# Kernel tuning notes

Measured on AMD Instinct MI355X. Metric: run time of the kernel, lower is better.

## Reference

```python
import jax, jax.numpy as jnp
import numpy as np

CLIP_MIN = 0.0
CLIP_MAX = 1.0
B, T, F, E, CD = 64, 48, 128, 64, 32


def setup_inputs() -> dict:
    key = jax.random.key(0)
    ks = jax.random.split(key, 8)
    return {
        "input_x": jax.random.uniform(ks[0], (B, T, F), dtype=jnp.float32),
        "mask": jax.random.randint(ks[1], (B, T, F), 0, 2, dtype=jnp.int32),
        "embed0": jax.random.normal(ks[2], (F, E), dtype=jnp.float32) * 0.1,
        "embed1": jax.random.normal(ks[3], (F, E), dtype=jnp.float32) * 0.1,
        "embed_missing": jax.random.normal(ks[4], (F, E), dtype=jnp.float32) * 0.1,
        "attention_f_w": jax.random.normal(ks[5], (F, E), dtype=jnp.float32) * 0.1,
        "attention_f_b": jnp.zeros((F,), dtype=jnp.float32),
        "compress_w": jax.random.normal(ks[6], (2 * E, CD), dtype=jnp.float32) * 0.1,
    }


def reference(input_x, mask, embed0, embed1, embed_missing, attention_f_w, attention_f_b, compress_w):
    b, t, f = input_x.shape
    # new_mask: feature observed anywhere in time -> [b, 1, f, 1] (broadcasts over time)
    m = (jnp.sum(mask, axis=-2) != 0).astype(input_x.dtype)[:, None, :, None]
    x = input_x[..., None]  # [b, t, f, 1]
    # interval embedding c: [b, t, f, e]
    c0 = (x - m * CLIP_MIN) * embed0
    c1 = (m * CLIP_MAX - x) * embed1
    c = (c0 + c1) / (CLIP_MAX - CLIP_MIN) + (1.0 - m) * embed_missing
    # pairwise scores: sum_e c_i * c_j * w_i + b_i  (avoids [b,t,f,f,e] materialization)
    scores = jnp.einsum("btie,btje->btij", c * attention_f_w, c) + attention_f_b[:, None]
    scores = jnp.clip(scores, -5.0, 5.0)
    off_diag = 1.0 - jnp.eye(f, dtype=c.dtype)
    masked_exps = jnp.exp(scores) * off_diag
    attn = masked_exps / (jnp.sum(masked_exps, axis=-1, keepdims=True) + 1e-8)  # [b,t,f,f]
    # weighted aggregation: sum_j attn_ij * (c_i * c_j) = c_i * (attn @ c)_i
    agg = c * jnp.einsum("btij,btje->btie", attn, c)
    a = jax.nn.relu(jnp.concatenate([c, agg], axis=-1))  # [b,t,f,2e]
    out = jnp.einsum("btfk,kd->btfd", a, compress_w)
    return out.reshape(b, t, f * compress_w.shape[-1])
```

## Files before the change

kernel.cpp:

```cpp
#include <hip/hip_runtime.h>

#define NB 64
#define NT 48
#define NF 128
#define NE 64
#define NCD 32

#define LOG2E 1.4426950408889634f

typedef __attribute__((ext_vector_type(8))) short bf16x8;
typedef __attribute__((ext_vector_type(4))) float f32x4;
typedef __attribute__((ext_vector_type(2))) uint u32x2;

#define WS_MFLAG 0
#define WS_DB    32768
#define WS_E1B   49152
#define WS_EMB   65536
#define WS_WLB   81920
#define WS_WT    98304
#define WS_BL    106496

__device__ __forceinline__ ushort f2bf(float x) {
    union { float f; uint u; } v; v.f = x;
    uint r = v.u + 0x7fffu + ((v.u >> 16) & 1u);
    return (ushort)(r >> 16);
}
__device__ __forceinline__ uint pk_bf16(float lo, float hi) {
    uint r; asm("v_cvt_pk_bf16_f32 %0, %1, %2" : "=v"(r) : "v"(lo), "v"(hi)); return r;
}
__device__ __forceinline__ float bflo(uint u) { union { uint u; float f; } v; v.u = u << 16; return v.f; }
__device__ __forceinline__ float bfhi(uint u) { union { uint u; float f; } v; v.u = u & 0xffff0000u; return v.f; }
__device__ __forceinline__ float exp2i(float x) { float r; asm("v_exp_f32 %0, %1" : "=v"(r) : "v"(x)); return r; }
__device__ __forceinline__ float rcpi(float x)  { float r; asm("v_rcp_f32 %0, %1" : "=v"(r) : "v"(x)); return r; }

#define TRR(dst, addr, IMM) \
    asm volatile("ds_read_b64_tr_b16 %0, %1 offset:" IMM : "=v"(dst) : "v"(addr))
#define PLSWAP(a, b) asm("v_permlane32_swap_b32 %0, %1" : "+v"(a), "+v"(b))

#define AGG_ISSUE(CR, TB, O0, O1, O2, O3, O4, O5, O6, O7) \
    TRR(CR[0], TB, O0); TRR(CR[1], TB, O1); \
    TRR(CR[2], TB, O2); TRR(CR[3], TB, O3); \
    TRR(CR[4], TB, O4); TRR(CR[5], TB, O5); \
    TRR(CR[6], TB, O6); TRR(CR[7], TB, O7); \
    __builtin_amdgcn_sched_barrier(0);

#define AGG_CONSUME(CR, PF, AG) { \
    union { u32x2 d[2]; bf16x8 v; } q0, q1, q2, q3; \
    q0.d[0] = CR[0]; q0.d[1] = CR[1]; q1.d[0] = CR[2]; q1.d[1] = CR[3]; \
    q2.d[0] = CR[4]; q2.d[1] = CR[5]; q3.d[0] = CR[6]; q3.d[1] = CR[7]; \
    AG[0] = __builtin_amdgcn_mfma_f32_16x16x32_bf16(q0.v, PF, AG[0], 0, 0, 0); \
    AG[1] = __builtin_amdgcn_mfma_f32_16x16x32_bf16(q1.v, PF, AG[1], 0, 0, 0); \
    AG[2] = __builtin_amdgcn_mfma_f32_16x16x32_bf16(q2.v, PF, AG[2], 0, 0, 0); \
    AG[3] = __builtin_amdgcn_mfma_f32_16x16x32_bf16(q3.v, PF, AG[3], 0, 0, 0); }

#define PF_BUILD(PF, PP, KS) { \
    uint X0 = PP[4*(KS)], X1 = PP[4*(KS)+1], X2 = PP[4*(KS)+2], X3 = PP[4*(KS)+3]; \
    PLSWAP(X0, X2); PLSWAP(X1, X3); \
    PF.u[0] = X0; PF.u[1] = X1; PF.u[2] = X2; PF.u[3] = X3; }

#define LGKM_WAIT(N) \
    asm volatile("s_waitcnt lgkmcnt(" #N ")" ::: "memory"); \
    __builtin_amdgcn_sched_barrier(0);

__global__ __launch_bounds__(256) void prep_kernel(
    const int* __restrict__ mask, const float* __restrict__ e0, const float* __restrict__ e1,
    const float* __restrict__ em, const float* __restrict__ aw, const float* __restrict__ ab,
    const float* __restrict__ cw,
    uint* __restrict__ mflag, ushort* __restrict__ db, ushort* __restrict__ e1b,
    ushort* __restrict__ emb, ushort* __restrict__ wlb, ushort* __restrict__ wt,
    float* __restrict__ bl)
{
    const int blk = blockIdx.x, tid = threadIdx.x;
    if (blk < 32) {
        int idx = blk * 256 + tid;
        float e1v = e1[idx];
        e1b[idx] = f2bf(e1v);
        emb[idx] = f2bf(em[idx]);
        db[idx]  = f2bf(e0[idx] - e1v);
        wlb[idx] = f2bf(aw[idx] * LOG2E);
    } else if (blk < 64) {
        int idx = (blk - 32) * 256 + tid;
        int b = idx >> 7, f = idx & 127;
        const int* p = mask + b * (NT * NF) + f;
        int s = 0;
#pragma unroll
        for (int t = 0; t < NT; ++t) s += p[t * NF];
        mflag[idx] = (s != 0) ? 1u : 0u;
    } else if (blk < 80) {
        int idx = (blk - 64) * 256 + tid;
        int k = idx >> 5, d = idx & 31;
        int kd;
        if (k < 64) kd = k;
        else {
            int kk = k - 64;
            kd = 64 + ((kk & 51) | ((kk & 4) << 1) | ((kk & 8) >> 1));
        }
        wt[d * 128 + kd] = f2bf(cw[idx]);
    } else {
        if (tid < NF) bl[tid] = ab[tid] * LOG2E;
    }
}

__global__ __launch_bounds__(512, 6) void fused_kernel(
    const float* __restrict__ input_x, const uint* __restrict__ mflag,
    const ushort* __restrict__ db, const ushort* __restrict__ e1b, const ushort* __restrict__ emb,
    const ushort* __restrict__ wlb, const float* __restrict__ blog,
    const ushort* __restrict__ wt, float* __restrict__ out)
{
    __shared__ ushort sC[2 * 9248];

    const int tid = threadIdx.x;
    const int blk = blockIdx.x;
    const int b   = blk / 24;
    const int bt0 = b * NT + (blk % 24) * 2;
    const int bt1 = bt0 + 1;

    const int wv = tid >> 6, ln = tid & 63;
    const int lr = ln & 15, lg = ln >> 4;
    const int i0 = wv << 4, irow = i0 + lr;

    const float bl = blog[irow];
    const float x0 = input_x[bt0 * NF + irow];
    const float x1 = input_x[bt1 * NF + irow];
    const ushort* Mrow = (mflag[b * NF + irow] ? e1b : emb) + irow * NE;
    const ushort* Drow = db + irow * NE;
    const ushort* Wrow = wlb + irow * NE;

    const int sbase = (lg >> 1) * 2312 + (lr >> 2) * 72 + (lr & 3) * 16 + (lg & 1) * 8;

    ushort* sC0 = sC;
    ushort* sC1 = sC + 9248;

    bf16x8 cwf0[2];
#pragma unroll
    for (int ks = 0; ks < 2; ++ks) {
        const int eo = ks * 32 + lg * 8;
        uint d4[4], m4[4], w4[4];
        *(uint4*)d4 = *(const uint4*)(Drow + eo);
        *(uint4*)m4 = *(const uint4*)(Mrow + eo);
        *(uint4*)w4 = *(const uint4*)(Wrow + eo);
        uint cb0[4], cb1[4];
        union { uint u[4]; bf16x8 v; } cw0;
#pragma unroll
        for (int j = 0; j < 4; ++j) {
            float dlo = bflo(d4[j]), dhi = bfhi(d4[j]);
            float mlo = bflo(m4[j]), mhi = bfhi(m4[j]);
            float c0lo = fmaf(x0, dlo, mlo), c0hi = fmaf(x0, dhi, mhi);
            float c1lo = fmaf(x1, dlo, mlo), c1hi = fmaf(x1, dhi, mhi);
            cb0[j] = pk_bf16(c0lo, c0hi);
            cb1[j] = pk_bf16(c1lo, c1hi);
            cw0.u[j] = pk_bf16(c0lo * bflo(w4[j]), c0hi * bfhi(w4[j]));
        }
        cwf0[ks] = cw0.v;
        *(uint4*)&sC0[sbase + wv * 288 + ks * 4624] = *(uint4*)cb0;
        *(uint4*)&sC1[sbase + wv * 288 + ks * 4624] = *(uint4*)cb1;
    }
    __syncthreads();

    auto run_S4 = [&](const ushort* base, bf16x8 w0, bf16x8 w1, int jt0, f32x4* st4) {
#pragma unroll
        for (int j = 0; j < 4; ++j) {
            const int jt = jt0 + j;
            f32x4 a = (f32x4){bl, bl, bl, bl};
            bf16x8 a0 = *(bf16x8*)&base[sbase + jt * 288];
            a = __builtin_amdgcn_mfma_f32_16x16x32_bf16(a0, w0, a, 0, 0, 0);
            bf16x8 a1 = *(bf16x8*)&base[sbase + jt * 288 + 4624];
            a = __builtin_amdgcn_mfma_f32_16x16x32_bf16(a1, w1, a, 0, 0, 0);
            st4[j] = a;
        }
    };
    auto run_SM4 = [&](f32x4* st4, uint* pp, int jt0, float* rsa) {
#pragma unroll
        for (int j = 0; j < 4; ++j) {
            const int jt = jt0 + j;
            f32x4 v = st4[j];
            float e0 = exp2i(v[0]);
            float e1 = exp2i(v[1]);
            float e2 = exp2i(v[2]);
            float e3 = exp2i(v[3]);
            if (jt == wv) {
                const bool on = (lg == (lr >> 2));
                e0 = (on && (lr & 3) == 0) ? 0.f : e0;
                e1 = (on && (lr & 3) == 1) ? 0.f : e1;
                e2 = (on && (lr & 3) == 2) ? 0.f : e2;
                e3 = (on && (lr & 3) == 3) ? 0.f : e3;
            }
            rsa[0] += e0; rsa[1] += e1; rsa[2] += e2; rsa[3] += e3;
            pp[2 * jt]     = pk_bf16(e0, e1);
            pp[2 * jt + 1] = pk_bf16(e2, e3);
        }
    };
    auto run_chain = [&](const ushort* base, bf16x8 w0, bf16x8 w1, int bt) {
        uint pp[16];
        float inv;
        {
            f32x4 st4[4];
            float rsa[4] = {0.f, 0.f, 0.f, 0.f};
            run_S4(base, w0, w1, 0, st4);
            run_SM4(st4, pp, 0, rsa);
            run_S4(base, w0, w1, 4, st4);
            run_SM4(st4, pp, 4, rsa);
            float rs = (rsa[0] + rsa[1]) + (rsa[2] + rsa[3]);
            rs += __shfl_xor(rs, 16);
            rs += __shfl_xor(rs, 32);
            inv = rcpi(rs + 1e-8f);
        }
        f32x4 ag[4];
#pragma unroll
        for (int et = 0; et < 4; ++et) ag[et] = (f32x4){0.f, 0.f, 0.f, 0.f};
        {
            const uint tb = (uint)(uintptr_t)base
                          + 2u * (uint)(72 * (((lg >> 1) << 2) + (lg & 1)) + lr);
            u32x2 cA[8];
            union { uint u[4]; bf16x8 v; } pf;
            LGKM_WAIT(0);
            PF_BUILD(pf, pp, 0);
            AGG_ISSUE(cA, tb, "0", "144", "4624", "4768", "9248", "9392", "13872", "14016");
            LGKM_WAIT(0);  AGG_CONSUME(cA, pf.v, ag);
            PF_BUILD(pf, pp, 1);
            AGG_ISSUE(cA, tb, "1152", "1296", "5776", "5920", "10400", "10544", "15024", "15168");
            LGKM_WAIT(0);  AGG_CONSUME(cA, pf.v, ag);
            PF_BUILD(pf, pp, 2);
            AGG_ISSUE(cA, tb, "2304", "2448", "6928", "7072", "11552", "11696", "16176", "16320");
            LGKM_WAIT(0);  AGG_CONSUME(cA, pf.v, ag);
            PF_BUILD(pf, pp, 3);
            AGG_ISSUE(cA, tb, "3456", "3600", "8080", "8224", "12704", "12848", "17328", "17472");
            LGKM_WAIT(0);  AGG_CONSUME(cA, pf.v, ag);
        }
        uint aa[8];
        {
            const int ebase = (wv * 4 + (lr >> 2)) * 72 + (lr & 3) * 16 + lg * 4;
#pragma unroll
            for (int et = 0; et < 4; ++et) {
                u32x2 cb2 = *(u32x2*)&base[ebase + et * 2312];
                float a0f = fmaxf(ag[et][0] * inv * bflo(cb2.x), 0.f);
                float a1f = fmaxf(ag[et][1] * inv * bfhi(cb2.x), 0.f);
                float a2f = fmaxf(ag[et][2] * inv * bflo(cb2.y), 0.f);
                float a3f = fmaxf(ag[et][3] * inv * bfhi(cb2.y), 0.f);
                aa[2 * et]     = pk_bf16(a0f, a1f);
                aa[2 * et + 1] = pk_bf16(a2f, a3f);
            }
        }
        f32x4 oc[2];
        oc[0] = (f32x4){0.f, 0.f, 0.f, 0.f};
        oc[1] = (f32x4){0.f, 0.f, 0.f, 0.f};
#pragma unroll
        for (int ks = 0; ks < 4; ++ks) {
            bf16x8 wfa = *(const bf16x8*)(wt + lr * 128 + ks * 32 + lg * 8);
            bf16x8 wfb = *(const bf16x8*)(wt + (16 + lr) * 128 + ks * 32 + lg * 8);
            bf16x8 afr;
            if (ks < 2) {
                const uint4 cc = *(uint4*)&base[sbase + wv * 288 + ks * 4624];
                union { uint u[4]; bf16x8 v; } rl;
                asm("v_pk_max_i16 %0, %1, 0" : "=v"(rl.u[0]) : "v"(cc.x));
                asm("v_pk_max_i16 %0, %1, 0" : "=v"(rl.u[1]) : "v"(cc.y));
                asm("v_pk_max_i16 %0, %1, 0" : "=v"(rl.u[2]) : "v"(cc.z));
                asm("v_pk_max_i16 %0, %1, 0" : "=v"(rl.u[3]) : "v"(cc.w));
                afr = rl.v;
            } else {
                const int kk = ks - 2;
                uint Y0 = aa[4 * kk], Y1 = aa[4 * kk + 1], Y2 = aa[4 * kk + 2], Y3 = aa[4 * kk + 3];
                PLSWAP(Y0, Y2);
                PLSWAP(Y1, Y3);
                union { uint u[4]; bf16x8 v; } af;
                af.u[0] = Y0; af.u[1] = Y1; af.u[2] = Y2; af.u[3] = Y3;
                afr = af.v;
            }
            oc[0] = __builtin_amdgcn_mfma_f32_16x16x32_bf16(afr, wfa, oc[0], 0, 0, 0);
            oc[1] = __builtin_amdgcn_mfma_f32_16x16x32_bf16(afr, wfb, oc[1], 0, 0, 0);
        }
        float* op = out + bt * (NF * NCD);
#pragma unroll
        for (int dt = 0; dt < 2; ++dt)
#pragma unroll
            for (int r = 0; r < 4; ++r)
                op[(i0 + lg * 4 + r) * NCD + dt * 16 + lr] = oc[dt][r];
    };

    run_chain(sC0, cwf0[0], cwf0[1], bt0);

    bf16x8 cwf1[2];
#pragma unroll
    for (int ks = 0; ks < 2; ++ks) {
        bf16x8 cf = *(bf16x8*)&sC1[sbase + wv * 288 + ks * 4624];
        uint w4[4];
        *(uint4*)w4 = *(const uint4*)(Wrow + ks * 32 + lg * 8);
        const uint* cu = (const uint*)&cf;
        union { uint u[4]; bf16x8 v; } cwu;
#pragma unroll
        for (int j = 0; j < 4; ++j)
            cwu.u[j] = pk_bf16(bflo(cu[j]) * bflo(w4[j]), bfhi(cu[j]) * bfhi(w4[j]));
        cwf1[ks] = cwu.v;
    }

    run_chain(sC1, cwf1[0], cwf1[1], bt1);
}

extern "C" void kernel_launch(void* const* d_in, const int* in_sizes, int n_in,
                              void* d_out, int out_size, void* d_ws, size_t ws_size,
                              hipStream_t stream) {
    const float* input_x       = (const float*)d_in[0];
    const int*   mask          = (const int*)d_in[1];
    const float* embed0        = (const float*)d_in[2];
    const float* embed1        = (const float*)d_in[3];
    const float* embed_missing = (const float*)d_in[4];
    const float* attn_w        = (const float*)d_in[5];
    const float* attn_b        = (const float*)d_in[6];
    const float* compress_w    = (const float*)d_in[7];
    float* out = (float*)d_out;

    char* ws = (char*)d_ws;
    uint*   mflag = (uint*)(ws + WS_MFLAG);
    ushort* dbp   = (ushort*)(ws + WS_DB);
    ushort* e1bp  = (ushort*)(ws + WS_E1B);
    ushort* embp  = (ushort*)(ws + WS_EMB);
    ushort* wlbp  = (ushort*)(ws + WS_WLB);
    ushort* wtp   = (ushort*)(ws + WS_WT);
    float*  blp   = (float*)(ws + WS_BL);

    hipLaunchKernelGGL(prep_kernel, dim3(81), dim3(256), 0, stream,
                       mask, embed0, embed1, embed_missing, attn_w, attn_b, compress_w,
                       mflag, dbp, e1bp, embp, wlbp, wtp, blp);
    hipLaunchKernelGGL(fused_kernel, dim3(NB * NT / 2), dim3(512), 0, stream,
                       input_x, mflag, dbp, e1bp, embp, wlbp, blp, wtp, out);
}
```

Before: 48.92 us.

## Interleave score/softmax chunks with aggregation MFMAs using software-pipelined LDS reads

Restructures the attention chain so the score MFMAs, exp and pack for each pair of j-tiles run chunk by chunk, interleaved with the aggregation MFMAs. Explicit ds_read_b128 and transposed reads are issued ahead under partial lgkmcnt waits, so LDS latency overlaps compute. Normalization is deferred until after aggregation. Occupancy hint drops from 6 to 4 waves per SIMD to give room for the extra live registers, which may reduce latency hiding across waves.

```diff
diff --git a/kernel.cpp b/kernel.cpp
--- a/kernel.cpp
+++ b/kernel.cpp
@@ -35,6 +35,8 @@
 
 #define TRR(dst, addr, IMM) \
     asm volatile("ds_read_b64_tr_b16 %0, %1 offset:" IMM : "=v"(dst) : "v"(addr))
+#define SRD(dst, addr, IMM) \
+    asm volatile("ds_read_b128 %0, %1 offset:" IMM : "=v"(dst) : "v"(addr))
 #define PLSWAP(a, b) asm("v_permlane32_swap_b32 %0, %1" : "+v"(a), "+v"(b))
 
 #define AGG_ISSUE(CR, TB, O0, O1, O2, O3, O4, O5, O6, O7) \
@@ -42,6 +44,11 @@
     TRR(CR[2], TB, O2); TRR(CR[3], TB, O3); \
     TRR(CR[4], TB, O4); TRR(CR[5], TB, O5); \
     TRR(CR[6], TB, O6); TRR(CR[7], TB, O7); \
+    __builtin_amdgcn_sched_barrier(0);
+
+#define SRD_ISSUE(SD, AB, O0, O1, O2, O3) \
+    SRD(SD[0], AB, O0); SRD(SD[1], AB, O1); \
+    SRD(SD[2], AB, O2); SRD(SD[3], AB, O3); \
     __builtin_amdgcn_sched_barrier(0);
 
 #define AGG_CONSUME(CR, PF, AG) { \
@@ -52,11 +59,6 @@
     AG[1] = __builtin_amdgcn_mfma_f32_16x16x32_bf16(q1.v, PF, AG[1], 0, 0, 0); \
     AG[2] = __builtin_amdgcn_mfma_f32_16x16x32_bf16(q2.v, PF, AG[2], 0, 0, 0); \
     AG[3] = __builtin_amdgcn_mfma_f32_16x16x32_bf16(q3.v, PF, AG[3], 0, 0, 0); }
-
-#define PF_BUILD(PF, PP, KS) { \
-    uint X0 = PP[4*(KS)], X1 = PP[4*(KS)+1], X2 = PP[4*(KS)+2], X3 = PP[4*(KS)+3]; \
-    PLSWAP(X0, X2); PLSWAP(X1, X3); \
-    PF.u[0] = X0; PF.u[1] = X1; PF.u[2] = X2; PF.u[3] = X3; }
 
 #define LGKM_WAIT(N) \
     asm volatile("s_waitcnt lgkmcnt(" #N ")" ::: "memory"); \
@@ -101,7 +103,7 @@
     }
 }
 
-__global__ __launch_bounds__(512, 6) void fused_kernel(
+__global__ __launch_bounds__(512, 4) void fused_kernel(
     const float* __restrict__ input_x, const uint* __restrict__ mflag,
     const ushort* __restrict__ db, const ushort* __restrict__ e1b, const ushort* __restrict__ emb,
     const ushort* __restrict__ wlb, const float* __restrict__ blog,
@@ -157,76 +159,82 @@
     }
     __syncthreads();
 
-    auto run_S4 = [&](const ushort* base, bf16x8 w0, bf16x8 w1, int jt0, f32x4* st4) {
-#pragma unroll
-        for (int j = 0; j < 4; ++j) {
-            const int jt = jt0 + j;
-            f32x4 a = (f32x4){bl, bl, bl, bl};
-            bf16x8 a0 = *(bf16x8*)&base[sbase + jt * 288];
-            a = __builtin_amdgcn_mfma_f32_16x16x32_bf16(a0, w0, a, 0, 0, 0);
-            bf16x8 a1 = *(bf16x8*)&base[sbase + jt * 288 + 4624];
-            a = __builtin_amdgcn_mfma_f32_16x16x32_bf16(a1, w1, a, 0, 0, 0);
-            st4[j] = a;
-        }
+    auto chunk = [&](const bf16x8* sd, bf16x8 w0, bf16x8 w1, int jt0, float* rsa,
+                     bf16x8* pfo) {
+        f32x4 s0 = (f32x4){bl, bl, bl, bl};
+        s0 = __builtin_amdgcn_mfma_f32_16x16x32_bf16(sd[0], w0, s0, 0, 0, 0);
+        s0 = __builtin_amdgcn_mfma_f32_16x16x32_bf16(sd[2], w1, s0, 0, 0, 0);
+        f32x4 s1 = (f32x4){bl, bl, bl, bl};
+        s1 = __builtin_amdgcn_mfma_f32_16x16x32_bf16(sd[1], w0, s1, 0, 0, 0);
+        s1 = __builtin_amdgcn_mfma_f32_16x16x32_bf16(sd[3], w1, s1, 0, 0, 0);
+        float e00 = exp2i(s0[0]), e01 = exp2i(s0[1]), e02 = exp2i(s0[2]), e03 = exp2i(s0[3]);
+        float e10 = exp2i(s1[0]), e11 = exp2i(s1[1]), e12 = exp2i(s1[2]), e13 = exp2i(s1[3]);
+        const bool on = (lg == (lr >> 2));
+        if (jt0 == wv) {
+            e00 = (on && (lr & 3) == 0) ? 0.f : e00;
+            e01 = (on && (lr & 3) == 1) ? 0.f : e01;
+            e02 = (on && (lr & 3) == 2) ? 0.f : e02;
+            e03 = (on && (lr & 3) == 3) ? 0.f : e03;
+        }
+        if (jt0 + 1 == wv) {
+            e10 = (on && (lr & 3) == 0) ? 0.f : e10;
+            e11 = (on && (lr & 3) == 1) ? 0.f : e11;
+            e12 = (on && (lr & 3) == 2) ? 0.f : e12;
+            e13 = (on && (lr & 3) == 3) ? 0.f : e13;
+        }
+        rsa[0] += e00 + e10; rsa[1] += e01 + e11;
+        rsa[2] += e02 + e12; rsa[3] += e03 + e13;
+        uint p0 = pk_bf16(e00, e01), p1 = pk_bf16(e02, e03);
+        uint p2 = pk_bf16(e10, e11), p3 = pk_bf16(e12, e13);
+        PLSWAP(p0, p2); PLSWAP(p1, p3);
+        union { uint u[4]; bf16x8 v; } pf;
+        pf.u[0] = p0; pf.u[1] = p1; pf.u[2] = p2; pf.u[3] = p3;
+        *pfo = pf.v;
     };
-    auto run_SM4 = [&](f32x4* st4, uint* pp, int jt0, float* rsa) {
-#pragma unroll
-        for (int j = 0; j < 4; ++j) {
-            const int jt = jt0 + j;
-            f32x4 v = st4[j];
-            float e0 = exp2i(v[0]);
-            float e1 = exp2i(v[1]);
-            float e2 = exp2i(v[2]);
-            float e3 = exp2i(v[3]);
-            if (jt == wv) {
-                const bool on = (lg == (lr >> 2));
-                e0 = (on && (lr & 3) == 0) ? 0.f : e0;
-                e1 = (on && (lr & 3) == 1) ? 0.f : e1;
-                e2 = (on && (lr & 3) == 2) ? 0.f : e2;
-                e3 = (on && (lr & 3) == 3) ? 0.f : e3;
-            }
-            rsa[0] += e0; rsa[1] += e1; rsa[2] += e2; rsa[3] += e3;
-            pp[2 * jt]     = pk_bf16(e0, e1);
-            pp[2 * jt + 1] = pk_bf16(e2, e3);
-        }
-    };
+
     auto run_chain = [&](const ushort* base, bf16x8 w0, bf16x8 w1, int bt) {
-        uint pp[16];
-        float inv;
-        {
-            f32x4 st4[4];
-            float rsa[4] = {0.f, 0.f, 0.f, 0.f};
-            run_S4(base, w0, w1, 0, st4);
-            run_SM4(st4, pp, 0, rsa);
-            run_S4(base, w0, w1, 4, st4);
-            run_SM4(st4, pp, 4, rsa);
-            float rs = (rsa[0] + rsa[1]) + (rsa[2] + rsa[3]);
-            rs += __shfl_xor(rs, 16);
-            rs += __shfl_xor(rs, 32);
-            inv = rcpi(rs + 1e-8f);
-        }
+        const uint ab = (uint)(uintptr_t)&base[sbase];
+        const uint tb = (uint)(uintptr_t)base
+                      + 2u * (uint)(72 * (((lg >> 1) << 2) + (lg & 1)) + lr);
+        bf16x8 sd0[4], sd1[4];
+        u32x2 c0[8], c1[8];
+        bf16x8 pf;
         f32x4 ag[4];
 #pragma unroll
         for (int et = 0; et < 4; ++et) ag[et] = (f32x4){0.f, 0.f, 0.f, 0.f};
-        {
-            const uint tb = (uint)(uintptr_t)base
-                          + 2u * (uint)(72 * (((lg >> 1) << 2) + (lg & 1)) + lr);
-            u32x2 cA[8];
-            union { uint u[4]; bf16x8 v; } pf;
-            LGKM_WAIT(0);
-            PF_BUILD(pf, pp, 0);
-            AGG_ISSUE(cA, tb, "0", "144", "4624", "4768", "9248", "9392", "13872", "14016");
-            LGKM_WAIT(0);  AGG_CONSUME(cA, pf.v, ag);
-            PF_BUILD(pf, pp, 1);
-            AGG_ISSUE(cA, tb, "1152", "1296", "5776", "5920", "10400", "10544", "15024", "15168");
-            LGKM_WAIT(0);  AGG_CONSUME(cA, pf.v, ag);
-            PF_BUILD(pf, pp, 2);
-            AGG_ISSUE(cA, tb, "2304", "2448", "6928", "7072", "11552", "11696", "16176", "16320");
-            LGKM_WAIT(0);  AGG_CONSUME(cA, pf.v, ag);
-            PF_BUILD(pf, pp, 3);
-            AGG_ISSUE(cA, tb, "3456", "3600", "8080", "8224", "12704", "12848", "17328", "17472");
-            LGKM_WAIT(0);  AGG_CONSUME(cA, pf.v, ag);
-        }
+        float rsa[4] = {0.f, 0.f, 0.f, 0.f};
+
+        LGKM_WAIT(0);
+        SRD_ISSUE(sd0, ab, "0", "576", "9248", "9824");
+        AGG_ISSUE(c0, tb, "0", "144", "4624", "4768", "9248", "9392", "13872", "14016");
+        LGKM_WAIT(8);
+        chunk(sd0, w0, w1, 0, rsa, &pf);
+        SRD_ISSUE(sd1, ab, "1152", "1728", "10400", "10976");
+        LGKM_WAIT(4);
+        AGG_CONSUME(c0, pf, ag);
+        AGG_ISSUE(c1, tb, "1152", "1296", "5776", "5920", "10400", "10544", "15024", "15168");
+        LGKM_WAIT(8);
+        chunk(sd1, w0, w1, 2, rsa, &pf);
+        SRD_ISSUE(sd0, ab, "2304", "2880", "11552", "12128");
+        LGKM_WAIT(4);
+        AGG_CONSUME(c1, pf, ag);
+        AGG_ISSUE(c0, tb, "2304", "2448", "6928", "7072", "11552", "11696", "16176", "16320");
+        LGKM_WAIT(8);
+        chunk(sd0, w0, w1, 4, rsa, &pf);
+        SRD_ISSUE(sd1, ab, "3456", "4032", "12704", "13280");
+        LGKM_WAIT(4);
+        AGG_CONSUME(c0, pf, ag);
+        AGG_ISSUE(c1, tb, "3456", "3600", "8080", "8224", "12704", "12848", "17328", "17472");
+        LGKM_WAIT(8);
+        chunk(sd1, w0, w1, 6, rsa, &pf);
+        LGKM_WAIT(0);
+        AGG_CONSUME(c1, pf, ag);
+
+        float rs = (rsa[0] + rsa[1]) + (rsa[2] + rsa[3]);
+        rs += __shfl_xor(rs, 16);
+        rs += __shfl_xor(rs, 32);
+        const float inv = rcpi(rs + 1e-8f);
+
         uint aa[8];
         {
             const int ebase = (wv * 4 + (lr >> 2)) * 72 + (lr & 3) * 16 + lg * 4;
```

Measured after the change: 50.03 us. 2.3% more time.
